# Kernel optimization log

Measured on AMD Instinct MI355X. Metric: run time of the kernel, lower is better.

Reference implementation:

```python
import jax, jax.numpy as jnp
import numpy as np

B, S, D, H = 4, 2048, 1024, 16
DK = D // H  # 64
EPS = 1e-6


def setup_inputs() -> dict:
    key = jax.random.key(0)
    ks = jax.random.split(key, 8)
    scale = 0.02
    return {
        "query": jax.random.normal(ks[0], (B, S, D), jnp.float32),
        "key": jax.random.normal(ks[1], (B, S, D), jnp.float32),
        "value": jax.random.normal(ks[2], (B, S, D), jnp.float32),
        "mask": jnp.zeros((B, 1, S, S), jnp.float32),  # additive mask
        "Wq": jax.random.normal(ks[3], (D, D), jnp.float32) * scale,
        "Wk": jax.random.normal(ks[4], (D, D), jnp.float32) * scale,
        "Wv": jax.random.normal(ks[5], (D, D), jnp.float32) * scale,
        "Wo": jax.random.normal(ks[6], (D, D), jnp.float32) * scale,
        "gamma": jnp.ones((D,), jnp.float32),
        "beta": jnp.zeros((D,), jnp.float32),
    }


def reference(query, key, value, mask, Wq, Wk, Wv, Wo, gamma, beta):
    residual = query
    # projections: [B,S,D] -> [B,H,S,dk]
    q = (query @ Wq).reshape(B, S, H, DK).transpose(0, 2, 1, 3)
    k = (key @ Wk).reshape(B, S, H, DK).transpose(0, 2, 1, 3)
    v = (value @ Wv).reshape(B, S, H, DK).transpose(0, 2, 1, 3)
    temperature = jnp.sqrt(jnp.asarray(DK, q.dtype))
    scores = jnp.einsum("bhqd,bhkd->bhqk", q, k) / temperature + mask
    p_attn = jax.nn.softmax(scores, axis=-1)  # dropout p=0 (eval)
    x = jnp.einsum("bhqk,bhkd->bhqd", p_attn, v)
    x = x.transpose(0, 2, 1, 3).reshape(B, S, D)
    x = x @ Wo
    y = residual + x
    mu = jnp.mean(y, axis=-1, keepdims=True)
    var = jnp.var(y, axis=-1, keepdims=True)
    return (y - mu) * jax.lax.rsqrt(var + EPS) * gamma + beta
```

## Files before the change

kernel.cpp:

```cpp
#include <hip/hip_runtime.h>
#include <string.h>

typedef unsigned short u16;
typedef unsigned int u32;
typedef __bf16 bf16x8 __attribute__((ext_vector_type(8)));
typedef float f32x4 __attribute__((ext_vector_type(4)));
typedef float f32x16 __attribute__((ext_vector_type(16)));
typedef u16 us8 __attribute__((ext_vector_type(8)));
typedef u16 us4 __attribute__((ext_vector_type(4)));
typedef u32 uu4 __attribute__((ext_vector_type(4)));

#define DEVINL __device__ __forceinline__

static constexpr int Bn = 4, Sn = 2048, Dn = 1024, Hn = 16;
static constexpr float LOG2E = 1.4426950408889634f;

DEVINL u16 f2bf(float f) {
  __bf16 h = (__bf16)f;
  u16 u;
  memcpy(&u, &h, 2);
  return u;
}

DEVINL void gload16(const void* g, void* l) {
  __builtin_amdgcn_global_load_lds((const __attribute__((address_space(1))) void*)g,
                                   (__attribute__((address_space(3))) void*)l, 16, 0, 0);
}

DEVINL unsigned swz(unsigned row, unsigned kbyte) {
  return row * 128u + (kbyte ^ ((row & 7u) << 4));
}

DEVINL bf16x8 lds8(const u16* base, unsigned byteoff) {
  return *(const bf16x8*)((const char*)base + byteoff);
}

DEVINL u32 cvtpk(float a, float b) {
  u32 r;
  asm("v_cvt_pk_bf16_f32 %0, %1, %2" : "=v"(r) : "v"(a), "v"(b));
  return r;
}

DEVINL void permswap(u32& x, u32& y) {
  asm("v_permlane32_swap_b32 %0, %1" : "+v"(x), "+v"(y));
}

__global__ __launch_bounds__(256) void cvt_all(const float* __restrict__ q, const float* __restrict__ k,
                                               const float* __restrict__ v, const float* __restrict__ mask,
                                               u16* __restrict__ oq, u16* __restrict__ ok,
                                               u16* __restrict__ ov, int* __restrict__ flag) {
  int z = blockIdx.y;
  if (z == 3) {
    size_t i = ((size_t)blockIdx.x * 256 + threadIdx.x) * 4;
    float4 m = *(const float4*)(mask + i);
    bool nz = (m.x != 0.f) || (m.y != 0.f) || (m.z != 0.f) || (m.w != 0.f);
    if (nz) atomicOr(flag, 1);
    return;
  }
  const float* in = z == 0 ? q : (z == 1 ? k : v);
  u16* out = z == 0 ? oq : (z == 1 ? ok : ov);
  size_t i = ((size_t)blockIdx.x * 256 + threadIdx.x) * 8;
  float4 a = *(const float4*)(in + i);
  float4 b = *(const float4*)(in + i + 4);
  us8 o;
  o[0] = f2bf(a.x); o[1] = f2bf(a.y); o[2] = f2bf(a.z); o[3] = f2bf(a.w);
  o[4] = f2bf(b.x); o[5] = f2bf(b.y); o[6] = f2bf(b.z); o[7] = f2bf(b.w);
  *(us8*)(out + i) = o;
}

__global__ __launch_bounds__(256) void cvt_w_all(const float* __restrict__ w0, const float* __restrict__ w1,
                                                 const float* __restrict__ w2, const float* __restrict__ w3,
                                                 u16* __restrict__ t0, u16* __restrict__ t1,
                                                 u16* __restrict__ t2, u16* __restrict__ t3) {
  int z = blockIdx.z;
  const float* W = z == 0 ? w0 : (z == 1 ? w1 : (z == 2 ? w2 : w3));
  u16* Wt = z == 0 ? t0 : (z == 1 ? t1 : (z == 2 ? t2 : t3));
  __shared__ float T[32][33];
  int n0 = blockIdx.x * 32, k0 = blockIdx.y * 32;
  int tx = threadIdx.x & 31, ty = threadIdx.x >> 5;
#pragma unroll
  for (int r = 0; r < 4; r++)
    T[ty + r * 8][tx] = W[(size_t)(k0 + ty + r * 8) * 1024 + n0 + tx];
  __syncthreads();
#pragma unroll
  for (int r = 0; r < 4; r++)
    Wt[(size_t)(n0 + ty + r * 8) * 1024 + k0 + tx] = f2bf(T[tx][ty + r * 8]);
}

__global__ __launch_bounds__(256) void transpose_v(const u16* __restrict__ V, u16* __restrict__ Vt) {
  __shared__ u16 T[64][72];
  int s0 = blockIdx.x * 64;
  int b = blockIdx.y >> 4, h = blockIdx.y & 15;
  int tid = threadIdx.x;
#pragma unroll
  for (int it = 0; it < 2; it++) {
    int chunk = it * 256 + tid;
    int s = chunk >> 3, c = chunk & 7;
    us8 v = *(const us8*)&V[((size_t)(b * Sn + s0 + s)) * Dn + h * 64 + c * 8];
#pragma unroll
    for (int j = 0; j < 8; j++) T[c * 8 + j][s] = v[j];
  }
  __syncthreads();
#pragma unroll
  for (int it = 0; it < 2; it++) {
    int chunk = it * 256 + tid;
    int dk = chunk >> 3, c = chunk & 7;
    us8 o = *(const us8*)&T[dk][c * 8];
    *(us8*)&Vt[((size_t)((b * Hn + h) * 64 + dk)) * Sn + s0 + c * 8] = o;
  }
}

template <int EPI>
DEVINL void gemm_body(const u16* __restrict__ A, const u16* __restrict__ Bt, void* __restrict__ Cout,
                      const float* __restrict__ resid, float alpha, u16* As, u16* Bs, int m0, int n0) {
  constexpr int K = 1024, N = 1024;
  int tid = threadIdx.x, w = tid >> 6, l = tid & 63;
  int wr = w >> 1, wc = w & 1;
  int l15 = l & 15, l4 = l >> 4;
  int lrow8 = l >> 3;
  int chunk = (l & 7) ^ (lrow8 & 7);

  f32x4 acc[4][4];
#pragma unroll
  for (int i = 0; i < 4; i++)
#pragma unroll
    for (int j = 0; j < 4; j++)
#pragma unroll
      for (int r = 0; r < 4; r++) acc[i][j][r] = 0.f;

  for (int kt = 0; kt < K; kt += 64) {
    __syncthreads();
#pragma unroll
    for (int c = 0; c < 4; c++) {
      int rowb = w * 32 + c * 8;
      int row = rowb + lrow8;
      gload16(&A[(size_t)(m0 + row) * K + kt + chunk * 8], &As[rowb * 64]);
      gload16(&Bt[(size_t)(n0 + row) * K + kt + chunk * 8], &Bs[rowb * 64]);
    }
    __syncthreads();
#pragma unroll
    for (int kk = 0; kk < 2; kk++) {
      bf16x8 af[4], bfr[4];
#pragma unroll
      for (int i = 0; i < 4; i++) {
        af[i] = lds8(As, swz(wr * 64 + i * 16 + l15, kk * 64 + l4 * 16));
        bfr[i] = lds8(Bs, swz(wc * 64 + i * 16 + l15, kk * 64 + l4 * 16));
      }
#pragma unroll
      for (int mi = 0; mi < 4; mi++)
#pragma unroll
        for (int ni = 0; ni < 4; ni++)
          acc[mi][ni] = __builtin_amdgcn_mfma_f32_16x16x32_bf16(af[mi], bfr[ni], acc[mi][ni], 0, 0, 0);
    }
  }

#pragma unroll
  for (int mi = 0; mi < 4; mi++)
#pragma unroll
    for (int ni = 0; ni < 4; ni++)
#pragma unroll
      for (int r = 0; r < 4; r++) {
        int row = m0 + wr * 64 + mi * 16 + l4 * 4 + r;
        int col = n0 + wc * 64 + ni * 16 + l15;
        float v = acc[mi][ni][r] * alpha;
        if constexpr (EPI == 0) {
          ((u16*)Cout)[(size_t)row * N + col] = f2bf(v);
        } else {
          ((float*)Cout)[(size_t)row * N + col] = v + resid[(size_t)row * N + col];
        }
      }
}

DEVINL void swizzled_tiles(int& m0, int& n0) {
  int lin = blockIdx.y * 8 + blockIdx.x;
  int sl = (lin & 7) * 64 + (lin >> 3);
  n0 = (sl & 7) * 128;
  m0 = (sl >> 3) * 128;
}

__global__ __launch_bounds__(256) void gemm_qkv(const u16* __restrict__ Aq, const u16* __restrict__ Ak,
                                                const u16* __restrict__ Av, const u16* __restrict__ Wtq,
                                                const u16* __restrict__ Wtk, const u16* __restrict__ Wtv,
                                                u16* __restrict__ Cq, u16* __restrict__ Ck,
                                                u16* __restrict__ Cv, float alphaq) {
  __shared__ u16 As[128 * 64];
  __shared__ u16 Bs[128 * 64];
  int z = blockIdx.z;
  const u16* A = z == 0 ? Aq : (z == 1 ? Ak : Av);
  const u16* Bt = z == 0 ? Wtq : (z == 1 ? Wtk : Wtv);
  u16* C = z == 0 ? Cq : (z == 1 ? Ck : Cv);
  float alpha = z == 0 ? alphaq : 1.0f;
  int m0, n0;
  swizzled_tiles(m0, n0);
  gemm_body<0>(A, Bt, C, nullptr, alpha, As, Bs, m0, n0);
}

__global__ __launch_bounds__(256) void gemm_o(const u16* __restrict__ A, const u16* __restrict__ Bt,
                                              float* __restrict__ Cout, const float* __restrict__ resid) {
  __shared__ u16 As[128 * 64];
  __shared__ u16 Bs[128 * 64];
  int m0, n0;
  swizzled_tiles(m0, n0);
  gemm_body<1>(A, Bt, Cout, resid, 1.0f, As, Bs, m0, n0);
}

__global__ __launch_bounds__(256) void attn_k(const u16* __restrict__ Qb, const u16* __restrict__ Kb,
                                              const u16* __restrict__ Vt, const float* __restrict__ mask,
                                              const int* __restrict__ flag, u16* __restrict__ Ob) {
  __shared__ u16 Ks[2][64 * 64];
  __shared__ u16 Vs[2][64 * 64];
  int tid = threadIdx.x, w = tid >> 6, l = tid & 63;
  int l31 = l & 31, hi = l >> 5;
  int b = blockIdx.y >> 4, h = blockIdx.y & 15;
  int q0 = blockIdx.x * 128;
  int lrow8 = l >> 3;
  int chunk = (l & 7) ^ (lrow8 & 7);

  bf16x8 qf[4];
  {
    const u16* qp = &Qb[((size_t)(b * Sn + q0 + w * 32 + l31)) * Dn + h * 64 + hi * 8];
#pragma unroll
    for (int ks = 0; ks < 4; ks++) qf[ks] = *(const bf16x8*)(qp + ks * 16);
  }

  float run_s = 0.f;
  f32x16 acc[2];
#pragma unroll
  for (int dt = 0; dt < 2; dt++)
#pragma unroll
    for (int r = 0; r < 16; r++) acc[dt][r] = 0.f;

  int msk = *flag;

  const u16* kptr = Kb + (size_t)b * Sn * Dn + h * 64 + chunk * 8;
  const u16* vptr = Vt + (size_t)(b * Hn + h) * 64 * Sn + chunk * 8;

#define STAGE(BUF)                                                    \
  {                                                                   \
    _Pragma("unroll") for (int c = 0; c < 2; c++) {                   \
      int rowb = w * 16 + c * 8;                                      \
      int kv = rowb + lrow8;                                          \
      gload16(kptr + (size_t)kv * Dn, &Ks[BUF][rowb * 64]);           \
      gload16(vptr + (size_t)kv * Sn, &Vs[BUF][rowb * 64]);           \
    }                                                                 \
  }

  STAGE(0);
  kptr += (size_t)64 * Dn;
  vptr += 64;
  int buf = 0;

  for (int t = 0; t < 32; t++) {
    __syncthreads();
    if (t + 1 < 32) {
      STAGE(buf ^ 1);
      kptr += (size_t)64 * Dn;
      vptr += 64;
    }

    f32x16 sc[2];
#pragma unroll
    for (int kvt = 0; kvt < 2; kvt++)
#pragma unroll
      for (int r = 0; r < 16; r++) sc[kvt][r] = 0.f;
#pragma unroll
    for (int ks = 0; ks < 4; ks++) {
#pragma unroll
      for (int kvt = 0; kvt < 2; kvt++) {
        bf16x8 kf = lds8(Ks[buf], swz(kvt * 32 + l31, ks * 32 + hi * 16));
        sc[kvt] = __builtin_amdgcn_mfma_f32_32x32x16_bf16(kf, qf[ks], sc[kvt], 0, 0, 0);
      }
    }

    if (msk) {
      const float* mp = &mask[((size_t)b * Sn + (q0 + w * 32 + l31)) * Sn + t * 64];
#pragma unroll
      for (int kvt = 0; kvt < 2; kvt++)
#pragma unroll
        for (int r = 0; r < 16; r++) {
          int kvl = (r & 3) + 8 * (r >> 2) + 4 * hi;
          sc[kvt][r] += mp[kvt * 32 + kvl] * LOG2E;
        }
    }

#pragma unroll
    for (int kvt = 0; kvt < 2; kvt++)
#pragma unroll
      for (int r = 0; r < 16; r++) {
        float p = exp2f(sc[kvt][r]);
        run_s += p;
        sc[kvt][r] = p;
      }

    bf16x8 pa[4];
#pragma unroll
    for (int ks = 0; ks < 4; ks++) {
      const f32x16& s = sc[ks >> 1];
      int rb = (ks & 1) * 8;
      u32 x0 = cvtpk(s[rb + 0], s[rb + 1]);
      u32 y0 = cvtpk(s[rb + 4], s[rb + 5]);
      u32 x1 = cvtpk(s[rb + 2], s[rb + 3]);
      u32 y1 = cvtpk(s[rb + 6], s[rb + 7]);
      permswap(x0, y0);
      permswap(x1, y1);
      uu4 wv;
      wv[0] = x0; wv[1] = x1; wv[2] = y0; wv[3] = y1;
      pa[ks] = *(bf16x8*)&wv;
    }

#pragma unroll
    for (int ks = 0; ks < 4; ks++) {
#pragma unroll
      for (int dt = 0; dt < 2; dt++) {
        bf16x8 vf = lds8(Vs[buf], swz(dt * 32 + l31, ks * 32 + hi * 16));
        acc[dt] = __builtin_amdgcn_mfma_f32_32x32x16_bf16(pa[ks], vf, acc[dt], 0, 0, 0);
      }
    }
    buf ^= 1;
  }
#undef STAGE

  run_s += __shfl_xor(run_s, 32);
  float inv = 1.0f / run_s;
#pragma unroll
  for (int r = 0; r < 16; r++) {
    int ql = (r & 3) + 8 * (r >> 2) + 4 * hi;
    float invq = __shfl(inv, ql);
    int row = q0 + w * 32 + ql;
#pragma unroll
    for (int dt = 0; dt < 2; dt++) {
      int col = h * 64 + dt * 32 + l31;
      Ob[((size_t)(b * Sn + row)) * Dn + col] = f2bf(acc[dt][r] * invq);
    }
  }
}

__global__ __launch_bounds__(256) void ln_k(const float* __restrict__ y, const float* __restrict__ gamma,
                                            const float* __restrict__ beta, float* __restrict__ out) {
  int row = blockIdx.x;
  int tid = threadIdx.x;
  const float* p = y + (size_t)row * 1024 + tid * 4;
  float4 v = *(const float4*)p;
  float s = v.x + v.y + v.z + v.w;
  float ss = v.x * v.x + v.y * v.y + v.z * v.z + v.w * v.w;
#pragma unroll
  for (int off = 1; off < 64; off <<= 1) {
    s += __shfl_xor(s, off);
    ss += __shfl_xor(ss, off);
  }
  __shared__ float rs_[4], rss_[4];
  int w = tid >> 6, l = tid & 63;
  if (l == 0) { rs_[w] = s; rss_[w] = ss; }
  __syncthreads();
  s = rs_[0] + rs_[1] + rs_[2] + rs_[3];
  ss = rss_[0] + rss_[1] + rss_[2] + rss_[3];
  float mean = s * (1.f / 1024.f);
  float var = ss * (1.f / 1024.f) - mean * mean;
  float rstd = rsqrtf(var + 1e-6f);
  float4 g = *(const float4*)(gamma + tid * 4);
  float4 bb = *(const float4*)(beta + tid * 4);
  float4 o;
  o.x = (v.x - mean) * rstd * g.x + bb.x;
  o.y = (v.y - mean) * rstd * g.y + bb.y;
  o.z = (v.z - mean) * rstd * g.z + bb.z;
  o.w = (v.w - mean) * rstd * g.w + bb.w;
  *(float4*)(out + (size_t)row * 1024 + tid * 4) = o;
}

extern "C" void kernel_launch(void* const* d_in, const int* in_sizes, int n_in,
                              void* d_out, int out_size, void* d_ws, size_t ws_size,
                              hipStream_t stream) {
  const float* query = (const float*)d_in[0];
  const float* key_ = (const float*)d_in[1];
  const float* value = (const float*)d_in[2];
  const float* mask = (const float*)d_in[3];
  const float* Wq = (const float*)d_in[4];
  const float* Wk = (const float*)d_in[5];
  const float* Wv = (const float*)d_in[6];
  const float* Wo = (const float*)d_in[7];
  const float* gamma = (const float*)d_in[8];
  const float* beta = (const float*)d_in[9];

  char* ws = (char*)d_ws;
  int* flag = (int*)ws;
  size_t off = 256;
  u16* Wtq = (u16*)(ws + off); off += (size_t)1024 * 1024 * 2;
  u16* Wtk = (u16*)(ws + off); off += (size_t)1024 * 1024 * 2;
  u16* Wtv = (u16*)(ws + off); off += (size_t)1024 * 1024 * 2;
  u16* Wto = (u16*)(ws + off); off += (size_t)1024 * 1024 * 2;
  const size_t TOK = (size_t)8192 * 1024;
  u16* Qb = (u16*)(ws + off); off += TOK * 2;
  u16* Kb = (u16*)(ws + off); off += TOK * 2;
  u16* Vb = (u16*)(ws + off); off += TOK * 2;
  u16* Vt = (u16*)(ws + off); off += TOK * 2;
  u16* Xq = (u16*)(ws + off); off += TOK * 2;
  u16* Xk = (u16*)(ws + off); off += TOK * 2;
  u16* Xv = (u16*)(ws + off); off += TOK * 2;
  u16* attnX = Xq;
  float* yb = (float*)Xk;

  hipMemsetAsync(flag, 0, 4, stream);

  cvt_all<<<dim3(4096, 4), 256, 0, stream>>>(query, key_, value, mask, Xq, Xk, Xv, flag);
  cvt_w_all<<<dim3(32, 32, 4), 256, 0, stream>>>(Wq, Wk, Wv, Wo, Wtq, Wtk, Wtv, Wto);

  gemm_qkv<<<dim3(8, 64, 3), 256, 0, stream>>>(Xq, Xk, Xv, Wtq, Wtk, Wtv, Qb, Kb, Vb,
                                               0.125f * LOG2E);

  transpose_v<<<dim3(32, 64), 256, 0, stream>>>(Vb, Vt);

  attn_k<<<dim3(16, 64), 256, 0, stream>>>(Qb, Kb, Vt, mask, flag, attnX);

  gemm_o<<<dim3(8, 64), 256, 0, stream>>>(attnX, Wto, yb, query);

  ln_k<<<8192, 256, 0, stream>>>(yb, gamma, beta, (float*)d_out);
}
```

Measured before the change: 426.6 us.

## Split attention KV range across two wave groups and compute row sums via MFMA

The attention kernel now launches 512 threads. Two groups of four waves each handle alternating 64-key tiles for the same 128 queries, and their partial outputs and row sums are merged through shared memory at the end. Row sums are now computed with an MFMA against a ones vector instead of scalar adds and shuffles. The software double-buffered prefetch is replaced by a load-then-sync pattern with two barriers per iteration. That exposes load latency and adds a reduction epilogue, in exchange for more waves per block.

```diff
diff --git a/kernel.cpp b/kernel.cpp
--- a/kernel.cpp
+++ b/kernel.cpp
@@ -204,12 +204,13 @@
   gemm_body<1>(A, Bt, Cout, resid, 1.0f, As, Bs, m0, n0);
 }
 
-__global__ __launch_bounds__(256) void attn_k(const u16* __restrict__ Qb, const u16* __restrict__ Kb,
-                                              const u16* __restrict__ Vt, const float* __restrict__ mask,
-                                              const int* __restrict__ flag, u16* __restrict__ Ob) {
+__global__ __launch_bounds__(512, 4) void attn_k(const u16* __restrict__ Qb, const u16* __restrict__ Kb,
+                                                 const u16* __restrict__ Vt, const float* __restrict__ mask,
+                                                 const int* __restrict__ flag, u16* __restrict__ Ob) {
   __shared__ u16 Ks[2][64 * 64];
   __shared__ u16 Vs[2][64 * 64];
   int tid = threadIdx.x, w = tid >> 6, l = tid & 63;
+  int qg = w & 3, p = w >> 2;
   int l31 = l & 31, hi = l >> 5;
   int b = blockIdx.y >> 4, h = blockIdx.y & 15;
   int q0 = blockIdx.x * 128;
@@ -218,119 +219,139 @@
 
   bf16x8 qf[4];
   {
-    const u16* qp = &Qb[((size_t)(b * Sn + q0 + w * 32 + l31)) * Dn + h * 64 + hi * 8];
+    const u16* qp = &Qb[((size_t)(b * Sn + q0 + qg * 32 + l31)) * Dn + h * 64 + hi * 8];
 #pragma unroll
     for (int ks = 0; ks < 4; ks++) qf[ks] = *(const bf16x8*)(qp + ks * 16);
   }
 
-  float run_s = 0.f;
+  bf16x8 ones;
+  {
+    us8 o1;
+#pragma unroll
+    for (int i = 0; i < 8; i++) o1[i] = 0x3F80;
+    ones = *(bf16x8*)&o1;
+  }
+
   f32x16 acc[2];
+  f32x16 acc_s;
 #pragma unroll
   for (int dt = 0; dt < 2; dt++)
 #pragma unroll
     for (int r = 0; r < 16; r++) acc[dt][r] = 0.f;
+#pragma unroll
+  for (int r = 0; r < 16; r++) acc_s[r] = 0.f;
 
   int msk = *flag;
 
-  const u16* kptr = Kb + (size_t)b * Sn * Dn + h * 64 + chunk * 8;
-  const u16* vptr = Vt + (size_t)(b * Hn + h) * 64 * Sn + chunk * 8;
-
-#define STAGE(BUF)                                                    \
-  {                                                                   \
-    _Pragma("unroll") for (int c = 0; c < 2; c++) {                   \
-      int rowb = w * 16 + c * 8;                                      \
-      int kv = rowb + lrow8;                                          \
-      gload16(kptr + (size_t)kv * Dn, &Ks[BUF][rowb * 64]);           \
-      gload16(vptr + (size_t)kv * Sn, &Vs[BUF][rowb * 64]);           \
-    }                                                                 \
-  }
-
-  STAGE(0);
-  kptr += (size_t)64 * Dn;
-  vptr += 64;
-  int buf = 0;
-
-  for (int t = 0; t < 32; t++) {
+  const size_t kbase = (size_t)b * Sn * Dn + h * 64 + chunk * 8;
+  const size_t vbase = (size_t)(b * Hn + h) * 64 * Sn + chunk * 8;
+  const float* mrow = mask + ((size_t)b * Sn + (q0 + qg * 32 + l31)) * Sn;
+
+  for (int j = 0; j < 16; j++) {
+    int kv0 = (2 * j + p) * 64;
     __syncthreads();
-    if (t + 1 < 32) {
-      STAGE(buf ^ 1);
-      kptr += (size_t)64 * Dn;
-      vptr += 64;
-    }
-
-    f32x16 sc[2];
-#pragma unroll
-    for (int kvt = 0; kvt < 2; kvt++)
-#pragma unroll
-      for (int r = 0; r < 16; r++) sc[kvt][r] = 0.f;
-#pragma unroll
-    for (int ks = 0; ks < 4; ks++) {
-#pragma unroll
-      for (int kvt = 0; kvt < 2; kvt++) {
-        bf16x8 kf = lds8(Ks[buf], swz(kvt * 32 + l31, ks * 32 + hi * 16));
-        sc[kvt] = __builtin_amdgcn_mfma_f32_32x32x16_bf16(kf, qf[ks], sc[kvt], 0, 0, 0);
-      }
-    }
-
-    if (msk) {
-      const float* mp = &mask[((size_t)b * Sn + (q0 + w * 32 + l31)) * Sn + t * 64];
-#pragma unroll
-      for (int kvt = 0; kvt < 2; kvt++)
+#pragma unroll
+    for (int c = 0; c < 2; c++) {
+      int rowb = qg * 16 + c * 8;
+      int kv = rowb + lrow8;
+      gload16(Kb + kbase + (size_t)(kv0 + kv) * Dn, &Ks[p][rowb * 64]);
+      gload16(Vt + vbase + (size_t)kv * Sn + kv0, &Vs[p][rowb * 64]);
+    }
+    __syncthreads();
+
+#pragma unroll
+    for (int kvt = 0; kvt < 2; kvt++) {
+      f32x16 sc;
+#pragma unroll
+      for (int r = 0; r < 16; r++) sc[r] = 0.f;
+#pragma unroll
+      for (int ks = 0; ks < 4; ks++) {
+        bf16x8 kf = lds8(Ks[p], swz(kvt * 32 + l31, ks * 32 + hi * 16));
+        sc = __builtin_amdgcn_mfma_f32_32x32x16_bf16(kf, qf[ks], sc, 0, 0, 0);
+      }
+
+      if (msk) {
+        const float* mp = mrow + kv0 + kvt * 32;
 #pragma unroll
         for (int r = 0; r < 16; r++) {
           int kvl = (r & 3) + 8 * (r >> 2) + 4 * hi;
-          sc[kvt][r] += mp[kvt * 32 + kvl] * LOG2E;
+          sc[r] += mp[kvl] * LOG2E;
         }
-    }
-
-#pragma unroll
-    for (int kvt = 0; kvt < 2; kvt++)
-#pragma unroll
-      for (int r = 0; r < 16; r++) {
-        float p = exp2f(sc[kvt][r]);
-        run_s += p;
-        sc[kvt][r] = p;
-      }
-
-    bf16x8 pa[4];
-#pragma unroll
-    for (int ks = 0; ks < 4; ks++) {
-      const f32x16& s = sc[ks >> 1];
-      int rb = (ks & 1) * 8;
-      u32 x0 = cvtpk(s[rb + 0], s[rb + 1]);
-      u32 y0 = cvtpk(s[rb + 4], s[rb + 5]);
-      u32 x1 = cvtpk(s[rb + 2], s[rb + 3]);
-      u32 y1 = cvtpk(s[rb + 6], s[rb + 7]);
-      permswap(x0, y0);
-      permswap(x1, y1);
-      uu4 wv;
-      wv[0] = x0; wv[1] = x1; wv[2] = y0; wv[3] = y1;
-      pa[ks] = *(bf16x8*)&wv;
-    }
-
-#pragma unroll
-    for (int ks = 0; ks < 4; ks++) {
+      }
+
+#pragma unroll
+      for (int r = 0; r < 16; r++) sc[r] = exp2f(sc[r]);
+
+      bf16x8 pa[2];
+#pragma unroll
+      for (int s = 0; s < 2; s++) {
+        int rb = s * 8;
+        u32 x0 = cvtpk(sc[rb + 0], sc[rb + 1]);
+        u32 y0 = cvtpk(sc[rb + 4], sc[rb + 5]);
+        u32 x1 = cvtpk(sc[rb + 2], sc[rb + 3]);
+        u32 y1 = cvtpk(sc[rb + 6], sc[rb + 7]);
+        permswap(x0, y0);
+        permswap(x1, y1);
+        uu4 wv;
+        wv[0] = x0; wv[1] = x1; wv[2] = y0; wv[3] = y1;
+        pa[s] = *(bf16x8*)&wv;
+      }
+
+      acc_s = __builtin_amdgcn_mfma_f32_32x32x16_bf16(pa[0], ones, acc_s, 0, 0, 0);
+      acc_s = __builtin_amdgcn_mfma_f32_32x32x16_bf16(pa[1], ones, acc_s, 0, 0, 0);
+
 #pragma unroll
       for (int dt = 0; dt < 2; dt++) {
-        bf16x8 vf = lds8(Vs[buf], swz(dt * 32 + l31, ks * 32 + hi * 16));
-        acc[dt] = __builtin_amdgcn_mfma_f32_32x32x16_bf16(pa[ks], vf, acc[dt], 0, 0, 0);
-      }
-    }
-    buf ^= 1;
-  }
-#undef STAGE
-
-  run_s += __shfl_xor(run_s, 32);
-  float inv = 1.0f / run_s;
-#pragma unroll
-  for (int r = 0; r < 16; r++) {
-    int ql = (r & 3) + 8 * (r >> 2) + 4 * hi;
-    float invq = __shfl(inv, ql);
-    int row = q0 + w * 32 + ql;
-#pragma unroll
-    for (int dt = 0; dt < 2; dt++) {
-      int col = h * 64 + dt * 32 + l31;
-      Ob[((size_t)(b * Sn + row)) * Dn + col] = f2bf(acc[dt][r] * invq);
+        bf16x8 vf0 = lds8(Vs[p], swz(dt * 32 + l31, (2 * kvt) * 32 + hi * 16));
+        bf16x8 vf1 = lds8(Vs[p], swz(dt * 32 + l31, (2 * kvt + 1) * 32 + hi * 16));
+        acc[dt] = __builtin_amdgcn_mfma_f32_32x32x16_bf16(pa[0], vf0, acc[dt], 0, 0, 0);
+        acc[dt] = __builtin_amdgcn_mfma_f32_32x32x16_bf16(pa[1], vf1, acc[dt], 0, 0, 0);
+      }
+    }
+  }
+
+  __syncthreads();
+  float* Xf = (float*)&Ks[0][0];
+  if (p == 1) {
+    float* a = Xf + qg * 1024;
+    float* c0 = Xf + 4096 + qg * 1024;
+#pragma unroll
+    for (int r = 0; r < 16; r++) {
+      a[r * 64 + l] = acc_s[r];
+      c0[r * 64 + l] = acc[0][r];
+    }
+  }
+  __syncthreads();
+  if (p == 0) {
+    const float* a = Xf + qg * 1024;
+    const float* c0 = Xf + 4096 + qg * 1024;
+#pragma unroll
+    for (int r = 0; r < 16; r++) {
+      acc_s[r] += a[r * 64 + l];
+      acc[0][r] += c0[r * 64 + l];
+    }
+  }
+  __syncthreads();
+  if (p == 1) {
+    float* c1 = Xf + qg * 1024;
+#pragma unroll
+    for (int r = 0; r < 16; r++) c1[r * 64 + l] = acc[1][r];
+  }
+  __syncthreads();
+  if (p == 0) {
+    const float* c1 = Xf + qg * 1024;
+#pragma unroll
+    for (int r = 0; r < 16; r++) acc[1][r] += c1[r * 64 + l];
+#pragma unroll
+    for (int r = 0; r < 16; r++) {
+      float inv = 1.0f / acc_s[r];
+      int ql = (r & 3) + 8 * (r >> 2) + 4 * hi;
+      int row = q0 + qg * 32 + ql;
+#pragma unroll
+      for (int dt = 0; dt < 2; dt++) {
+        int col = h * 64 + dt * 32 + l31;
+        Ob[((size_t)(b * Sn + row)) * Dn + col] = f2bf(acc[dt][r] * inv);
+      }
     }
   }
 }
@@ -409,7 +430,7 @@
 
   transpose_v<<<dim3(32, 64), 256, 0, stream>>>(Vb, Vt);
 
-  attn_k<<<dim3(16, 64), 256, 0, stream>>>(Qb, Kb, Vt, mask, flag, attnX);
+  attn_k<<<dim3(16, 64), 512, 0, stream>>>(Qb, Kb, Vt, mask, flag, attnX);
 
   gemm_o<<<dim3(8, 64), 256, 0, stream>>>(attnX, Wto, yb, query);
 
```

Result: faster. 404.7 us (-5.1%).
